# Kernel tuning notes

Measured on AMD Instinct MI355X. Metric: run time of the kernel, lower is better.

## Reference

```python
import jax, jax.numpy as jnp
import numpy as np

# Sizes (match input_specs)
B = 50                 # number of CRN graphs in the batch
NS_PER, NR_PER = 2000, 4000
N_S, N_R = B * NS_PER, B * NR_PER   # 100k species, 200k reactions total
E = 1_000_000          # bipartite edges
D = 128                # d_model
L = 2                  # n_layers
N_TYPES, P_DIM = 16, 8
MAX_SPECIES_IDX = 2000


def setup_inputs() -> dict:
    key = jax.random.key(0)
    ks = jax.random.split(key, 12)
    inp = {
        "species_indices": jax.random.randint(ks[0], (N_S,), 0, MAX_SPECIES_IDX, dtype=jnp.int32),
        "is_external": jax.random.randint(ks[1], (N_S,), 0, 2, dtype=jnp.int32),
        "propensity_type_ids": jax.random.randint(ks[2], (N_R,), 0, N_TYPES, dtype=jnp.int32),
        "propensity_params": jax.random.normal(ks[3], (N_R, P_DIM), dtype=jnp.float32),
        "edge_species": jax.random.randint(ks[4], (E,), 0, N_S, dtype=jnp.int32),
        "edge_reaction": jax.random.randint(ks[5], (E,), 0, N_R, dtype=jnp.int32),
        # contiguous per-graph segment ids (graphs are equal-sized)
        "species_batch": jnp.repeat(jnp.arange(B, dtype=jnp.int32), NS_PER),
        "reaction_batch": jnp.repeat(jnp.arange(B, dtype=jnp.int32), NR_PER),
        # learned parameters
        "species_table": jax.random.normal(ks[6], (MAX_SPECIES_IDX, D), dtype=jnp.float32) * 0.02,
        "external_table": jax.random.normal(ks[7], (2, D), dtype=jnp.float32) * 0.02,
        "type_table": jax.random.normal(ks[8], (N_TYPES, D), dtype=jnp.float32) * 0.02,
        "W_param": jax.random.normal(ks[9], (P_DIM, D), dtype=jnp.float32) * 0.1,
        "b_param": jnp.zeros((D,), dtype=jnp.float32),
        # per-layer message-passing weights: concat([h, msg]) -> d
        "Wr": jax.random.normal(ks[10], (L, 2 * D, D), dtype=jnp.float32) * 0.05,
        "br": jnp.zeros((L, D), dtype=jnp.float32),
        "Ws": jax.random.normal(ks[11], (L, 2 * D, D), dtype=jnp.float32) * 0.05,
        "bs": jnp.zeros((L, D), dtype=jnp.float32),
    }
    return inp


def reference(species_indices, is_external, propensity_type_ids, propensity_params,
              edge_species, edge_reaction, species_batch, reaction_batch,
              species_table, external_table, type_table, W_param, b_param,
              Wr, br, Ws, bs):
    # Initial embeddings
    h_s = species_table[species_indices] + external_table[is_external]          # (N_S, D)
    h_r = type_table[propensity_type_ids] + propensity_params @ W_param + b_param  # (N_R, D)

    n_s, n_r = h_s.shape[0], h_r.shape[0]
    # Alternating bipartite sum message passing (SumMessagePassingLayer)
    for l in range(Wr.shape[0]):
        m_r = jax.ops.segment_sum(h_s[edge_species], edge_reaction, num_segments=n_r)
        h_r = jax.nn.relu(jnp.concatenate([h_r, m_r], axis=-1) @ Wr[l] + br[l])
        m_s = jax.ops.segment_sum(h_r[edge_reaction], edge_species, num_segments=n_s)
        h_s = jax.nn.relu(jnp.concatenate([h_s, m_s], axis=-1) @ Ws[l] + bs[l])

    # Segment-mean pooling per graph (index_add then divide by counts)
    pooled_s = jax.ops.segment_sum(h_s, species_batch, num_segments=B) / float(NS_PER)
    pooled_r = jax.ops.segment_sum(h_r, reaction_batch, num_segments=B) / float(NR_PER)
    context = jnp.concatenate([pooled_s, pooled_r], axis=-1)  # (B, 2D); dropout p=0 -> identity
    return context
```

## Files before the change

kernel.cpp:

```cpp
#include <hip/hip_runtime.h>
#include <stdint.h>

#define NS 100000
#define NR 200000
#define EE 1000000
#define DD 128
#define NB 50
#define NSP 2000
#define NRP 4000
#define BSH 10
#define NBR 196
#define NBS 98
#define CHUNK 8192

typedef short bf16x8 __attribute__((ext_vector_type(8)));
typedef float f32x4 __attribute__((ext_vector_type(4)));
typedef float f32x2 __attribute__((ext_vector_type(2)));
typedef unsigned u32x4 __attribute__((ext_vector_type(4)));
typedef unsigned u32x2 __attribute__((ext_vector_type(2)));

__device__ __forceinline__ unsigned short f2bf(float f){
  unsigned u = __float_as_uint(f);
  u = (u + 0x7FFFu + ((u >> 16) & 1u)) >> 16;
  return (unsigned short)u;
}
__device__ __forceinline__ unsigned packbf(float a, float b){
  return (unsigned)f2bf(a) | ((unsigned)f2bf(b) << 16);
}
__device__ __forceinline__ float bflo(unsigned p){ return __uint_as_float(p << 16); }
__device__ __forceinline__ float bfhi(unsigned p){ return __uint_as_float(p & 0xFFFF0000u); }
__device__ __forceinline__ unsigned pack4fp8(float v0, float v1, float v2, float v3){
  unsigned p = __builtin_amdgcn_cvt_pk_fp8_f32(v0, v1, 0, false);
  p = __builtin_amdgcn_cvt_pk_fp8_f32(v2, v3, p, true);
  return p;
}

__global__ void pack_w(const float* __restrict__ Wr, const float* __restrict__ Ws,
                       unsigned short* __restrict__ Wp){
  int g = blockIdx.x*256 + threadIdx.x;
  if (g >= 4*32768) return;
  int j = g & 7; int rest = g >> 3;
  int lane = rest & 63; rest >>= 6;
  int ks = rest & 7; rest >>= 3;
  int ct = rest & 7; int mat = rest >> 3;
  int k  = ks*32 + (lane >> 4)*8 + j;
  int cc = ct*16 + (lane & 15);
  const float* src = (mat < 2) ? (Wr + (size_t)mat*256*DD) : (Ws + (size_t)(mat-2)*256*DD);
  Wp[g] = f2bf(src[(size_t)k*DD + cc]);
}

__global__ __launch_bounds__(256) void init_all(const int* __restrict__ si, const int* __restrict__ ext,
        const int* __restrict__ tid, const float* __restrict__ pp,
        const float* __restrict__ st, const float* __restrict__ et, const float* __restrict__ tt,
        const float* __restrict__ Wpar, const float* __restrict__ bpar,
        unsigned short* __restrict__ hs, unsigned short* __restrict__ hr,
        unsigned char* __restrict__ hs8){
  int g = blockIdx.x*256 + threadIdx.x;
  int row = g >> 4, colb = (g & 15) * 8;
  if (row < NS){
    const float* a = st + (size_t)si[row]*DD + colb;
    const float* b = et + (size_t)ext[row]*DD + colb;
    float4 x0 = ((const float4*)a)[0], x1 = ((const float4*)a)[1];
    float4 y0 = ((const float4*)b)[0], y1 = ((const float4*)b)[1];
    float s0 = x0.x+y0.x, s1 = x0.y+y0.y, s2 = x0.z+y0.z, s3 = x0.w+y0.w;
    float s4 = x1.x+y1.x, s5 = x1.y+y1.y, s6 = x1.z+y1.z, s7 = x1.w+y1.w;
    u32x4 o;
    o.x = packbf(s0, s1); o.y = packbf(s2, s3);
    o.z = packbf(s4, s5); o.w = packbf(s6, s7);
    *(u32x4*)(hs + (size_t)row*DD + colb) = o;
    u32x2 e; e.x = pack4fp8(s0, s1, s2, s3); e.y = pack4fp8(s4, s5, s6, s7);
    *(u32x2*)(hs8 + (size_t)row*DD + colb) = e;
  } else {
    int r = row - NS;
    const float* tb = tt + (size_t)tid[r]*DD + colb;
    float4 a0 = ((const float4*)tb)[0], a1 = ((const float4*)tb)[1];
    float4 b0 = ((const float4*)(bpar+colb))[0], b1 = ((const float4*)(bpar+colb))[1];
    a0.x += b0.x; a0.y += b0.y; a0.z += b0.z; a0.w += b0.w;
    a1.x += b1.x; a1.y += b1.y; a1.z += b1.z; a1.w += b1.w;
    const float* pr = pp + (size_t)r*8;
    float4 p0 = ((const float4*)pr)[0], p1 = ((const float4*)pr)[1];
    float w[8] = {p0.x,p0.y,p0.z,p0.w,p1.x,p1.y,p1.z,p1.w};
    #pragma unroll
    for (int p = 0; p < 8; p++){
      float4 w0 = ((const float4*)(Wpar + p*DD + colb))[0];
      float4 w1 = ((const float4*)(Wpar + p*DD + colb))[1];
      a0.x += w[p]*w0.x; a0.y += w[p]*w0.y; a0.z += w[p]*w0.z; a0.w += w[p]*w0.w;
      a1.x += w[p]*w1.x; a1.y += w[p]*w1.y; a1.z += w[p]*w1.z; a1.w += w[p]*w1.w;
    }
    u32x4 o;
    o.x = packbf(a0.x, a0.y); o.y = packbf(a0.z, a0.w);
    o.z = packbf(a1.x, a1.y); o.w = packbf(a1.z, a1.w);
    *(u32x4*)(hr + (size_t)r*DD + colb) = o;
  }
}

__global__ __launch_bounds__(256) void bucket_hist(const int* __restrict__ er, const int* __restrict__ es,
                                                   int* __restrict__ gcnt){
  __shared__ int cnt[NBR + NBS];
  int t = threadIdx.x;
  for (int j = t; j < NBR + NBS; j += 256) cnt[j] = 0;
  __syncthreads();
  long i0 = (long)blockIdx.x * 2048;
  for (int j = t; j < 2048; j += 256){
    long i = i0 + j;
    if (i < EE){
      atomicAdd(&cnt[er[i] >> BSH], 1);
      atomicAdd(&cnt[NBR + (es[i] >> BSH)], 1);
    }
  }
  __syncthreads();
  for (int j = t; j < NBR + NBS; j += 256)
    if (cnt[j]) atomicAdd(&gcnt[j], cnt[j]);
}

__global__ __launch_bounds__(256) void bucket_scan(const int* __restrict__ gcnt,
        int* __restrict__ bktOffR, int* __restrict__ bktOffS,
        int* __restrict__ gCurR, int* __restrict__ gCurS){
  __shared__ int a[256];
  int t = threadIdx.x;
  int own = (t < NBR) ? gcnt[t] : 0;
  a[t] = own; __syncthreads();
  for (int d = 1; d < 256; d <<= 1){
    int x = (t >= d) ? a[t-d] : 0;
    __syncthreads(); a[t] += x; __syncthreads();
  }
  if (t < NBR){ int v = a[t] - own; bktOffR[t] = v; gCurR[t] = v; }
  if (t == 0) bktOffR[NBR] = EE;
  __syncthreads();
  own = (t < NBS) ? gcnt[NBR + t] : 0;
  a[t] = own; __syncthreads();
  for (int d = 1; d < 256; d <<= 1){
    int x = (t >= d) ? a[t-d] : 0;
    __syncthreads(); a[t] += x; __syncthreads();
  }
  if (t < NBS){ int v = a[t] - own; bktOffS[t] = v; gCurS[t] = v; }
  if (t == 0) bktOffS[NBS] = EE;
}

__global__ __launch_bounds__(256) void bin_edges(const int* __restrict__ er, const int* __restrict__ es,
        int* __restrict__ gCurR, int* __restrict__ gCurS,
        unsigned* __restrict__ recR, unsigned* __restrict__ recS){
  __shared__ unsigned stage[CHUNK];
  __shared__ unsigned char stageb[CHUNK];
  __shared__ int cnt[256], scn[256], pref[256], gbase[256], lcur[256];
  int t = threadIdx.x;
  int side = blockIdx.y;
  const int* dest = side ? es : er;
  const int* srca = side ? er : es;
  int* gCur = side ? gCurS : gCurR;
  unsigned* rec = side ? recS : recR;
  int nbkt = side ? NBS : NBR;
  long i0 = (long)blockIdx.x * CHUNK;
  int n = (EE - i0 < CHUNK) ? (int)(EE - i0) : CHUNK;
  cnt[t] = 0;
  __syncthreads();
  for (int j = t; j < n; j += 256)
    atomicAdd(&cnt[dest[i0 + j] >> BSH], 1);
  __syncthreads();
  scn[t] = cnt[t];
  __syncthreads();
  for (int d = 1; d < 256; d <<= 1){
    int x = (t >= d) ? scn[t-d] : 0;
    __syncthreads(); scn[t] += x; __syncthreads();
  }
  pref[t] = scn[t] - cnt[t];
  lcur[t] = scn[t] - cnt[t];
  if (t < nbkt && cnt[t] > 0) gbase[t] = atomicAdd(&gCur[t], cnt[t]);
  __syncthreads();
  for (int j = t; j < n; j += 256){
    int d = dest[i0 + j];
    int s = srca[i0 + j];
    int b = d >> BSH;
    int p = atomicAdd(&lcur[b], 1);
    stage[p] = ((unsigned)(d - (b << BSH)) << 18) | (unsigned)s;
    stageb[p] = (unsigned char)b;
  }
  __syncthreads();
  for (int e = t; e < n; e += 256){
    int b = stageb[e];
    rec[gbase[b] + (e - pref[b])] = stage[e];
  }
}

__global__ __launch_bounds__(256) void build_csr(const unsigned* __restrict__ recR, const unsigned* __restrict__ recS,
        const int* __restrict__ bktOffR, const int* __restrict__ bktOffS,
        unsigned* __restrict__ csrR, unsigned* __restrict__ csrS,
        int* __restrict__ offsR, int* __restrict__ offsS){
  __shared__ int hist[1024], pref[1024], cur[1024], ws[256];
  int t = threadIdx.x;
  int bb = blockIdx.x;
  const unsigned* rec; const int* bktOff; unsigned* csr; int* offs; int N;
  if (bb < NBR){ rec = recR; bktOff = bktOffR; csr = csrR; offs = offsR; N = NR; }
  else { bb -= NBR; rec = recS; bktOff = bktOffS; csr = csrS; offs = offsS; N = NS; }
  int d0 = bb << BSH;
  int base = bktOff[bb], cnt_ = bktOff[bb+1] - base;
  #pragma unroll
  for (int j = 0; j < 4; j++) hist[t*4+j] = 0;
  __syncthreads();
  for (int e = t; e < cnt_; e += 256)
    atomicAdd(&hist[rec[base + e] >> 18], 1);
  __syncthreads();
  int s = 0, h[4];
  #pragma unroll
  for (int j = 0; j < 4; j++){ h[j] = hist[t*4+j]; s += h[j]; }
  ws[t] = s;
  __syncthreads();
  for (int d = 1; d < 256; d <<= 1){
    int x = (t >= d) ? ws[t-d] : 0;
    __syncthreads(); ws[t] += x; __syncthreads();
  }
  int run = ws[t] - s;
  #pragma unroll
  for (int j = 0; j < 4; j++){ pref[t*4+j] = run; cur[t*4+j] = base + run; run += h[j]; }
  __syncthreads();
  int DPB = N - d0; if (DPB > 1024) DPB = 1024;
  #pragma unroll
  for (int j = 0; j < 4; j++){
    int i = t*4 + j;
    if (i < DPB) offs[d0 + i] = base + pref[i];
  }
  if (t == 0 && d0 + DPB == N) offs[N] = EE;
  __syncthreads();
  for (int e = t; e < cnt_; e += 256){
    unsigned r = rec[base + e];
    int pos = atomicAdd(&cur[r >> 18], 1);
    csr[pos] = (((r >> 18) & 31u) << 26) | ((r & 0x3FFFFu) << 8);
  }
}

__global__ __launch_bounds__(256) void fused_layer(
        const unsigned char*  __restrict__ gsrc8,
        const unsigned short* __restrict__ hself,
        const int* __restrict__ offs, const unsigned* __restrict__ csr,
        const unsigned short* __restrict__ Wp, const float* __restrict__ bias,
        unsigned short* __restrict__ hout,
        unsigned char*  __restrict__ hout8)
{
  __shared__ unsigned short msgT[32*DD];
  int t = threadIdx.x;
  int lane = t & 63;
  int w = t >> 6;
  int quad = lane >> 4, rlo = lane & 15;
  int row0 = blockIdx.x * 32;

  {
    u32x4 z4 = {0u,0u,0u,0u};
    ((u32x4*)msgT)[w*128 + lane]      = z4;
    ((u32x4*)msgT)[w*128 + 64 + lane] = z4;
  }

  {
    int rbeg = row0 + w*8;
    int kp = __builtin_amdgcn_readfirstlane(offs[rbeg]);
    int ke = __builtin_amdgcn_readfirstlane(offs[rbeg + 8]);
    int c16 = lane >> 2, sub4 = lane & 3;
    const unsigned char* g8 = gsrc8;
    float a0 = 0.f, a1 = 0.f;
    int cur = -1;

    if (kp < ke){
      unsigned ra[8], rb[8], rcx[8];
      unsigned pa[8], pb[8], pc[8];

      #pragma unroll
      for (int i = 0; i < 8; i++){
        int kk;
        kk = kp + i;      if (kk > ke-1) kk = ke-1;
        ra[i]  = (unsigned)__builtin_amdgcn_readfirstlane(csr[kk]);
        kk = kp + 8 + i;  if (kk > ke-1) kk = ke-1;
        rb[i]  = (unsigned)__builtin_amdgcn_readfirstlane(csr[kk]);
        kk = kp + 16 + i; if (kk > ke-1) kk = ke-1;
        rcx[i] = (unsigned)__builtin_amdgcn_readfirstlane(csr[kk]);
      }
      #pragma unroll
      for (int i = 0; i < 8; i++)
        pa[i] = *(const unsigned short*)(g8 + ((ra[i] & 0x03FFFF00u) >> 1) + lane*2);
      #pragma unroll
      for (int i = 0; i < 8; i++)
        pb[i] = *(const unsigned short*)(g8 + ((rb[i] & 0x03FFFF00u) >> 1) + lane*2);

      auto process = [&](const unsigned* RC_, const unsigned* PV_){
        #pragma unroll
        for (int i = 0; i < 8; i++){
          if (kp + i < ke){
            int dl = (int)(RC_[i] >> 26);
            if (dl != cur){
              if (cur >= 0)
                *(unsigned*)(msgT + cur*DD + ((c16 ^ (cur & 7)) << 3) + (sub4 << 1)) = packbf(a0, a1);
              a0 = 0.f; a1 = 0.f;
              cur = dl;
            }
            f32x2 f = __builtin_amdgcn_cvt_pk_f32_fp8(PV_[i], false);
            a0 += f[0]; a1 += f[1];
          }
        }
      };

      while (true){
        if (kp >= ke) break;
        #pragma unroll
        for (int i = 0; i < 8; i++)
          pc[i] = *(const unsigned short*)(g8 + ((rcx[i] & 0x03FFFF00u) >> 1) + lane*2);
        process(ra, pa);
        #pragma unroll
        for (int i = 0; i < 8; i++){
          int kk = kp + 24 + i; if (kk > ke-1) kk = ke-1;
          ra[i] = (unsigned)__builtin_amdgcn_readfirstlane(csr[kk]);
        }
        kp += 8;

        if (kp >= ke) break;
        #pragma unroll
        for (int i = 0; i < 8; i++)
          pa[i] = *(const unsigned short*)(g8 + ((ra[i] & 0x03FFFF00u) >> 1) + lane*2);
        process(rb, pb);
        #pragma unroll
        for (int i = 0; i < 8; i++){
          int kk = kp + 24 + i; if (kk > ke-1) kk = ke-1;
          rb[i] = (unsigned)__builtin_amdgcn_readfirstlane(csr[kk]);
        }
        kp += 8;

        if (kp >= ke) break;
        #pragma unroll
        for (int i = 0; i < 8; i++)
          pb[i] = *(const unsigned short*)(g8 + ((rb[i] & 0x03FFFF00u) >> 1) + lane*2);
        process(rcx, pc);
        #pragma unroll
        for (int i = 0; i < 8; i++){
          int kk = kp + 24 + i; if (kk > ke-1) kk = ke-1;
          rcx[i] = (unsigned)__builtin_amdgcn_readfirstlane(csr[kk]);
        }
        kp += 8;
      }
      if (cur >= 0)
        *(unsigned*)(msgT + cur*DD + ((c16 ^ (cur & 7)) << 3) + (sub4 << 1)) = packbf(a0, a1);
    }
  }
  __syncthreads();

  int ct0 = w * 2;
  bf16x8 wf[16];
  #pragma unroll
  for (int ks = 0; ks < 8; ks++){
    wf[ks*2+0] = *(const bf16x8*)(Wp + (size_t)(((ct0+0)*8 + ks)*64 + lane) * 8);
    wf[ks*2+1] = *(const bf16x8*)(Wp + (size_t)(((ct0+1)*8 + ks)*64 + lane) * 8);
  }
  bf16x8 Hb0[4], Hb1[4];
  #pragma unroll
  for (int ks = 0; ks < 4; ks++){
    int kloc = ks*32 + quad*8;
    Hb0[ks] = *(const bf16x8*)(hself + (size_t)(row0 + rlo) * DD + kloc);
    Hb1[ks] = *(const bf16x8*)(hself + (size_t)(row0 + 16 + rlo) * DD + kloc);
  }
  bf16x8 Mb0[4], Mb1[4];
  #pragma unroll
  for (int ks2 = 0; ks2 < 4; ks2++){
    int c8 = ks2*4 + quad;
    int lr0 = rlo, lr1 = 16 + rlo;
    Mb0[ks2] = *(const bf16x8*)(msgT + lr0*DD + ((c8 ^ (lr0 & 7)) * 8));
    Mb1[ks2] = *(const bf16x8*)(msgT + lr1*DD + ((c8 ^ (lr1 & 7)) * 8));
  }

  f32x4 acc[2][2];
  #pragma unroll
  for (int i = 0; i < 2; i++)
    #pragma unroll
    for (int j = 0; j < 2; j++){ f32x4 z = {0.f,0.f,0.f,0.f}; acc[i][j] = z; }

  #pragma unroll
  for (int ks = 0; ks < 4; ks++){
    acc[0][0] = __builtin_amdgcn_mfma_f32_16x16x32_bf16(wf[ks*2+0], Hb0[ks], acc[0][0], 0, 0, 0);
    acc[0][1] = __builtin_amdgcn_mfma_f32_16x16x32_bf16(wf[ks*2+1], Hb0[ks], acc[0][1], 0, 0, 0);
    acc[1][0] = __builtin_amdgcn_mfma_f32_16x16x32_bf16(wf[ks*2+0], Hb1[ks], acc[1][0], 0, 0, 0);
    acc[1][1] = __builtin_amdgcn_mfma_f32_16x16x32_bf16(wf[ks*2+1], Hb1[ks], acc[1][1], 0, 0, 0);
  }
  #pragma unroll
  for (int ks2 = 0; ks2 < 4; ks2++){
    int ks = 4 + ks2;
    acc[0][0] = __builtin_amdgcn_mfma_f32_16x16x32_bf16(wf[ks*2+0], Mb0[ks2], acc[0][0], 0, 0, 0);
    acc[0][1] = __builtin_amdgcn_mfma_f32_16x16x32_bf16(wf[ks*2+1], Mb0[ks2], acc[0][1], 0, 0, 0);
    acc[1][0] = __builtin_amdgcn_mfma_f32_16x16x32_bf16(wf[ks*2+0], Mb1[ks2], acc[1][0], 0, 0, 0);
    acc[1][1] = __builtin_amdgcn_mfma_f32_16x16x32_bf16(wf[ks*2+1], Mb1[ks2], acc[1][1], 0, 0, 0);
  }

  #pragma unroll
  for (int c = 0; c < 2; c++){
    float4 bv = *(const float4*)(bias + (ct0+c)*16 + quad*4);
    #pragma unroll
    for (int rb = 0; rb < 2; rb++){
      int row = row0 + rb*16 + rlo;
      float v0 = acc[rb][c][0] + bv.x;
      float v1 = acc[rb][c][1] + bv.y;
      float v2 = acc[rb][c][2] + bv.z;
      float v3 = acc[rb][c][3] + bv.w;
      v0 = v0 > 0.f ? v0 : 0.f;
      v1 = v1 > 0.f ? v1 : 0.f;
      v2 = v2 > 0.f ? v2 : 0.f;
      v3 = v3 > 0.f ? v3 : 0.f;
      u32x2 o; o.x = packbf(v0, v1); o.y = packbf(v2, v3);
      *(u32x2*)(hout + (size_t)row*DD + (ct0+c)*16 + quad*4) = o;
      *(unsigned*)(hout8 + (size_t)row*DD + (ct0+c)*16 + quad*4) = pack4fp8(v0, v1, v2, v3);
    }
  }
}

__global__ __launch_bounds__(256) void pool(const unsigned short* __restrict__ hs,
        const unsigned short* __restrict__ hr, float* __restrict__ out){
  __shared__ float red[16][128];
  int b = blockIdx.x, part = blockIdx.y;
  int t = threadIdx.x;
  int rg = t >> 4, sub = t & 15;
  const unsigned short* src; int row0, outoff; float scale;
  if (part < 4){ src = hs; row0 = b*NSP + part*500; outoff = b*256; scale = 1.f/NSP; }
  else { src = hr; row0 = b*NRP + (part-4)*500; outoff = b*256 + 128; scale = 1.f/NRP; }
  float a0=0,a1=0,a2=0,a3=0,a4=0,a5=0,a6=0,a7=0;
  for (int r = rg; r < 500; r += 16){
    u32x4 p = *(const u32x4*)(src + (size_t)(row0+r)*DD + sub*8);
    a0 += bflo(p.x); a1 += bfhi(p.x);
    a2 += bflo(p.y); a3 += bfhi(p.y);
    a4 += bflo(p.z); a5 += bfhi(p.z);
    a6 += bflo(p.w); a7 += bfhi(p.w);
  }
  float* rr = &red[rg][sub*8];
  rr[0]=a0; rr[1]=a1; rr[2]=a2; rr[3]=a3; rr[4]=a4; rr[5]=a5; rr[6]=a6; rr[7]=a7;
  __syncthreads();
  if (t < 128){
    float s = 0.f;
    #pragma unroll
    for (int g = 0; g < 16; g++) s += red[g][t];
    atomicAdd(&out[outoff + t], s * scale);
  }
}

extern "C" void kernel_launch(void* const* d_in, const int* in_sizes, int n_in,
                              void* d_out, int out_size, void* d_ws, size_t ws_size,
                              hipStream_t stream)
{
  const int*   si   = (const int*)d_in[0];
  const int*   ext  = (const int*)d_in[1];
  const int*   tid  = (const int*)d_in[2];
  const float* pp   = (const float*)d_in[3];
  const int*   es   = (const int*)d_in[4];
  const int*   er   = (const int*)d_in[5];
  const float* st   = (const float*)d_in[8];
  const float* et   = (const float*)d_in[9];
  const float* tt   = (const float*)d_in[10];
  const float* Wpar = (const float*)d_in[11];
  const float* bpar = (const float*)d_in[12];
  const float* Wr   = (const float*)d_in[13];
  const float* br   = (const float*)d_in[14];
  const float* Ws   = (const float*)d_in[15];
  const float* bs   = (const float*)d_in[16];
  float* out = (float*)d_out;

  char* basep = (char*)d_ws; size_t off = 0;
  auto alloc = [&](size_t bytes)->char*{
    char* r = basep + off; off = (off + bytes + 255) & ~(size_t)255; return r;
  };
  unsigned short* hs0 = (unsigned short*)alloc((size_t)NS*DD*2);
  unsigned short* hs1 = (unsigned short*)alloc((size_t)NS*DD*2);
  unsigned short* hr0 = (unsigned short*)alloc((size_t)NR*DD*2);
  unsigned short* hr1 = (unsigned short*)alloc((size_t)NR*DD*2);
  unsigned short* Wp  = (unsigned short*)alloc((size_t)4*32768*2);
  int* offsR = (int*)alloc((size_t)(NR+1)*4);
  int* offsS = (int*)alloc((size_t)(NS+1)*4);
  unsigned* csrR = (unsigned*)alloc((size_t)EE*4);
  unsigned* csrS = (unsigned*)alloc((size_t)EE*4);
  unsigned char* f8S = (unsigned char*)alloc((size_t)NS*DD);
  unsigned char* f8R = (unsigned char*)alloc((size_t)NR*DD);
  int* gcnt   = (int*)alloc(2048);
  int* bktOffR= (int*)alloc(2048);
  int* bktOffS= (int*)alloc(2048);
  int* gCurR  = (int*)alloc(2048);
  int* gCurS  = (int*)alloc(2048);
  unsigned* recR = (unsigned*)hs1;
  unsigned* recS = (unsigned*)hr1;

  hipMemsetAsync(gcnt, 0, 2048, stream);
  hipMemsetAsync(d_out, 0, (size_t)out_size*4, stream);

  pack_w<<<512, 256, 0, stream>>>(Wr, Ws, Wp);
  init_all<<<(NS+NR)*16/256, 256, 0, stream>>>(si, ext, tid, pp, st, et, tt, Wpar, bpar, hs0, hr0, f8S);

  bucket_hist<<<(EE + 2047)/2048, 256, 0, stream>>>(er, es, gcnt);
  bucket_scan<<<1, 256, 0, stream>>>(gcnt, bktOffR, bktOffS, gCurR, gCurS);
  bin_edges<<<dim3((EE + CHUNK - 1)/CHUNK, 2), 256, 0, stream>>>(er, es, gCurR, gCurS, recR, recS);
  build_csr<<<NBR + NBS, 256, 0, stream>>>(recR, recS, bktOffR, bktOffS, csrR, csrS, offsR, offsS);

  fused_layer<<<NR/32, 256, 0, stream>>>(f8S, hr0, offsR, csrR, Wp + (size_t)0*32768, br + (size_t)0*DD, hr1, f8R);
  fused_layer<<<NS/32, 256, 0, stream>>>(f8R, hs0, offsS, csrS, Wp + (size_t)2*32768, bs + (size_t)0*DD, hs1, f8S);
  fused_layer<<<NR/32, 256, 0, stream>>>(f8S, hr1, offsR, csrR, Wp + (size_t)1*32768, br + (size_t)1*DD, hr0, f8R);
  fused_layer<<<NS/32, 256, 0, stream>>>(f8R, hs1, offsS, csrS, Wp + (size_t)3*32768, bs + (size_t)1*DD, hs0, f8S);

  pool<<<dim3(NB, 12), 256, 0, stream>>>(hs0, hr0, out);
}
```

Before: 470.4 us.

## Gather neighbor rows with 8 edges per wave in parallel and skip unused fp8 output

```diff
diff --git a/kernel.cpp b/kernel.cpp
--- a/kernel.cpp
+++ b/kernel.cpp
@@ -244,97 +244,56 @@
   int row0 = blockIdx.x * 32;
 
   {
-    u32x4 z4 = {0u,0u,0u,0u};
-    ((u32x4*)msgT)[w*128 + lane]      = z4;
-    ((u32x4*)msgT)[w*128 + 64 + lane] = z4;
-  }
-
-  {
+    int g = lane >> 3;
+    int s = lane & 7;
+    const unsigned char* g8 = gsrc8;
     int rbeg = row0 + w*8;
-    int kp = __builtin_amdgcn_readfirstlane(offs[rbeg]);
-    int ke = __builtin_amdgcn_readfirstlane(offs[rbeg + 8]);
-    int c16 = lane >> 2, sub4 = lane & 3;
-    const unsigned char* g8 = gsrc8;
-    float a0 = 0.f, a1 = 0.f;
-    int cur = -1;
-
-    if (kp < ke){
-      unsigned ra[8], rb[8], rcx[8];
-      unsigned pa[8], pb[8], pc[8];
-
-      #pragma unroll
-      for (int i = 0; i < 8; i++){
-        int kk;
-        kk = kp + i;      if (kk > ke-1) kk = ke-1;
-        ra[i]  = (unsigned)__builtin_amdgcn_readfirstlane(csr[kk]);
-        kk = kp + 8 + i;  if (kk > ke-1) kk = ke-1;
-        rb[i]  = (unsigned)__builtin_amdgcn_readfirstlane(csr[kk]);
-        kk = kp + 16 + i; if (kk > ke-1) kk = ke-1;
-        rcx[i] = (unsigned)__builtin_amdgcn_readfirstlane(csr[kk]);
+    #pragma unroll 1
+    for (int rr = 0; rr < 8; rr++){
+      int k  = __builtin_amdgcn_readfirstlane(offs[rbeg + rr]);
+      int ke = __builtin_amdgcn_readfirstlane(offs[rbeg + rr + 1]);
+      f32x2 p0_ = {0.f,0.f}, p1_ = {0.f,0.f}, p2_ = {0.f,0.f}, p3_ = {0.f,0.f};
+      f32x2 p4_ = {0.f,0.f}, p5_ = {0.f,0.f}, p6_ = {0.f,0.f}, p7_ = {0.f,0.f};
+      for (; k < ke; k += 8){
+        int kk = k + g;
+        unsigned rec = csr[kk < ke ? kk : (ke - 1)];
+        u32x4 d = *(const u32x4*)(g8 + ((rec & 0x03FFFF00u) >> 1) + s*16);
+        unsigned m4 = (kk < ke) ? 0xFFFFFFFFu : 0u;
+        d.x &= m4; d.y &= m4; d.z &= m4; d.w &= m4;
+        f32x2 f;
+        f = __builtin_amdgcn_cvt_pk_f32_fp8(d.x, false); p0_[0]+=f[0]; p0_[1]+=f[1];
+        f = __builtin_amdgcn_cvt_pk_f32_fp8(d.x, true ); p1_[0]+=f[0]; p1_[1]+=f[1];
+        f = __builtin_amdgcn_cvt_pk_f32_fp8(d.y, false); p2_[0]+=f[0]; p2_[1]+=f[1];
+        f = __builtin_amdgcn_cvt_pk_f32_fp8(d.y, true ); p3_[0]+=f[0]; p3_[1]+=f[1];
+        f = __builtin_amdgcn_cvt_pk_f32_fp8(d.z, false); p4_[0]+=f[0]; p4_[1]+=f[1];
+        f = __builtin_amdgcn_cvt_pk_f32_fp8(d.z, true ); p5_[0]+=f[0]; p5_[1]+=f[1];
+        f = __builtin_amdgcn_cvt_pk_f32_fp8(d.w, false); p6_[0]+=f[0]; p6_[1]+=f[1];
+        f = __builtin_amdgcn_cvt_pk_f32_fp8(d.w, true ); p7_[0]+=f[0]; p7_[1]+=f[1];
       }
       #pragma unroll
-      for (int i = 0; i < 8; i++)
-        pa[i] = *(const unsigned short*)(g8 + ((ra[i] & 0x03FFFF00u) >> 1) + lane*2);
-      #pragma unroll
-      for (int i = 0; i < 8; i++)
-        pb[i] = *(const unsigned short*)(g8 + ((rb[i] & 0x03FFFF00u) >> 1) + lane*2);
-
-      auto process = [&](const unsigned* RC_, const unsigned* PV_){
-        #pragma unroll
-        for (int i = 0; i < 8; i++){
-          if (kp + i < ke){
-            int dl = (int)(RC_[i] >> 26);
-            if (dl != cur){
-              if (cur >= 0)
-                *(unsigned*)(msgT + cur*DD + ((c16 ^ (cur & 7)) << 3) + (sub4 << 1)) = packbf(a0, a1);
-              a0 = 0.f; a1 = 0.f;
-              cur = dl;
-            }
-            f32x2 f = __builtin_amdgcn_cvt_pk_f32_fp8(PV_[i], false);
-            a0 += f[0]; a1 += f[1];
-          }
+      for (int msk = 8; msk <= 32; msk <<= 1){
+        p0_[0] += __shfl_xor(p0_[0], msk, 64); p0_[1] += __shfl_xor(p0_[1], msk, 64);
+        p1_[0] += __shfl_xor(p1_[0], msk, 64); p1_[1] += __shfl_xor(p1_[1], msk, 64);
+        p2_[0] += __shfl_xor(p2_[0], msk, 64); p2_[1] += __shfl_xor(p2_[1], msk, 64);
+        p3_[0] += __shfl_xor(p3_[0], msk, 64); p3_[1] += __shfl_xor(p3_[1], msk, 64);
+        p4_[0] += __shfl_xor(p4_[0], msk, 64); p4_[1] += __shfl_xor(p4_[1], msk, 64);
+        p5_[0] += __shfl_xor(p5_[0], msk, 64); p5_[1] += __shfl_xor(p5_[1], msk, 64);
+        p6_[0] += __shfl_xor(p6_[0], msk, 64); p6_[1] += __shfl_xor(p6_[1], msk, 64);
+        p7_[0] += __shfl_xor(p7_[0], msk, 64); p7_[1] += __shfl_xor(p7_[1], msk, 64);
+      }
+      if (g < 2){
+        u32x4 o;
+        if (g == 0){
+          o.x = packbf(p0_[0], p0_[1]); o.y = packbf(p1_[0], p1_[1]);
+          o.z = packbf(p2_[0], p2_[1]); o.w = packbf(p3_[0], p3_[1]);
+        } else {
+          o.x = packbf(p4_[0], p4_[1]); o.y = packbf(p5_[0], p5_[1]);
+          o.z = packbf(p6_[0], p6_[1]); o.w = packbf(p7_[0], p7_[1]);
         }
-      };
-
-      while (true){
-        if (kp >= ke) break;
-        #pragma unroll
-        for (int i = 0; i < 8; i++)
-          pc[i] = *(const unsigned short*)(g8 + ((rcx[i] & 0x03FFFF00u) >> 1) + lane*2);
-        process(ra, pa);
-        #pragma unroll
-        for (int i = 0; i < 8; i++){
-          int kk = kp + 24 + i; if (kk > ke-1) kk = ke-1;
-          ra[i] = (unsigned)__builtin_amdgcn_readfirstlane(csr[kk]);
-        }
-        kp += 8;
-
-        if (kp >= ke) break;
-        #pragma unroll
-        for (int i = 0; i < 8; i++)
-          pa[i] = *(const unsigned short*)(g8 + ((ra[i] & 0x03FFFF00u) >> 1) + lane*2);
-        process(rb, pb);
-        #pragma unroll
-        for (int i = 0; i < 8; i++){
-          int kk = kp + 24 + i; if (kk > ke-1) kk = ke-1;
-          rb[i] = (unsigned)__builtin_amdgcn_readfirstlane(csr[kk]);
-        }
-        kp += 8;
-
-        if (kp >= ke) break;
-        #pragma unroll
-        for (int i = 0; i < 8; i++)
-          pb[i] = *(const unsigned short*)(g8 + ((rb[i] & 0x03FFFF00u) >> 1) + lane*2);
-        process(rcx, pc);
-        #pragma unroll
-        for (int i = 0; i < 8; i++){
-          int kk = kp + 24 + i; if (kk > ke-1) kk = ke-1;
-          rcx[i] = (unsigned)__builtin_amdgcn_readfirstlane(csr[kk]);
-        }
-        kp += 8;
+        int lrow = w*8 + rr;
+        int chunk = (2*s + g) ^ (lrow & 7);
+        *(u32x4*)(msgT + (size_t)lrow*DD + chunk*8) = o;
       }
-      if (cur >= 0)
-        *(unsigned*)(msgT + cur*DD + ((c16 ^ (cur & 7)) << 3) + (sub4 << 1)) = packbf(a0, a1);
     }
   }
   __syncthreads();
@@ -400,7 +359,8 @@
       v3 = v3 > 0.f ? v3 : 0.f;
       u32x2 o; o.x = packbf(v0, v1); o.y = packbf(v2, v3);
       *(u32x2*)(hout + (size_t)row*DD + (ct0+c)*16 + quad*4) = o;
-      *(unsigned*)(hout8 + (size_t)row*DD + (ct0+c)*16 + quad*4) = pack4fp8(v0, v1, v2, v3);
+      if (hout8)
+        *(unsigned*)(hout8 + (size_t)row*DD + (ct0+c)*16 + quad*4) = pack4fp8(v0, v1, v2, v3);
     }
   }
 }
@@ -491,7 +451,7 @@
   fused_layer<<<NR/32, 256, 0, stream>>>(f8S, hr0, offsR, csrR, Wp + (size_t)0*32768, br + (size_t)0*DD, hr1, f8R);
   fused_layer<<<NS/32, 256, 0, stream>>>(f8R, hs0, offsS, csrS, Wp + (size_t)2*32768, bs + (size_t)0*DD, hs1, f8S);
   fused_layer<<<NR/32, 256, 0, stream>>>(f8S, hr1, offsR, csrR, Wp + (size_t)1*32768, br + (size_t)1*DD, hr0, f8R);
-  fused_layer<<<NS/32, 256, 0, stream>>>(f8R, hs1, offsS, csrS, Wp + (size_t)3*32768, bs + (size_t)1*DD, hs0, f8S);
+  fused_layer<<<NS/32, 256, 0, stream>>>(f8R, hs1, offsS, csrS, Wp + (size_t)3*32768, bs + (size_t)1*DD, hs0, (unsigned char*)nullptr);
 
   pool<<<dim3(NB, 12), 256, 0, stream>>>(hs0, hr0, out);
 }
```

Result: slower. 598.4 us (+27.2%).
